# Optimization experiments

Measured on AMD Instinct MI355X. Metric: run time of the kernel, lower is better.

The kernel has to match this reference:

```python
import jax, jax.numpy as jnp
import numpy as np

GROUP = 64  # hardcoded group_size in the module


def setup_inputs() -> dict:
    key = jax.random.key(0)
    ks = jax.random.split(key, 7)
    B, S, K, N, R = 64, 1, 4096, 12288, 32
    G = K // GROUP
    x = jax.random.normal(ks[0], (B, S, K), jnp.float32)
    # int4 weight residual values in [-8, 7]
    q_w = jax.random.randint(ks[1], (N, K), -8, 8, jnp.int32)
    # per-(group, out_channel) positive scales, shape [G, N] as in the module buffer
    wscales = jax.random.uniform(ks[2], (G, N), jnp.float32, 1e-3, 2e-2)
    lora_down = jax.random.normal(ks[3], (K, R), jnp.float32) * 0.02
    lora_up = jax.random.normal(ks[4], (N, R), jnp.float32) * 0.02
    smooth = jax.random.uniform(ks[5], (K,), jnp.float32, 0.5, 2.0)
    bias = jax.random.normal(ks[6], (N,), jnp.float32) * 0.01
    return {"x": x, "q_w": q_w, "wscales": wscales, "lora_down": lora_down,
            "lora_up": lora_up, "smooth": smooth, "bias": bias}


def reference(x, q_w, wscales, lora_down, lora_up, smooth, bias):
    # x: [B, S, K]; q_w: [N, K] int4 values; wscales: [K//64, N]
    B, S, K = x.shape
    G = K // GROUP
    # smoothing divide (per in-channel)
    x_div = x / smooth  # [B, S, K]
    # --- activation W4A4 path: symmetric int4 per-token per-group quantization ---
    xg = x_div.reshape(B, S, G, GROUP)
    ascale = jnp.maximum(jnp.max(jnp.abs(xg), axis=-1) / 7.0, 1e-8)  # [B, S, G]
    xq = jnp.clip(jnp.round(xg / ascale[..., None]), -8.0, 7.0)
    x_deq = (xq * ascale[..., None]).reshape(B, S, K)  # dequantized activation
    # --- dequantize int4 weight residual: w[n,k] = q[n,k] * wscales[k//64, n] ---
    w_deq = q_w.astype(jnp.float32) * jnp.repeat(wscales, GROUP, axis=0).T  # [N, K]
    # main quantized GEMM
    y = jnp.einsum('bsk,nk->bsn', x_deq, w_deq)  # [B, S, N]
    # low-rank SVD branch on the full-precision smoothed activation
    y = y + (x_div @ lora_down) @ lora_up.T
    y = y + bias
    return y
```

## Files before the change

kernel.cpp:

```cpp
#include <hip/hip_runtime.h>
#include <hip/hip_bf16.h>

#define K_DIM 4096
#define N_DIM 12288
#define B_DIM 64
#define G_DIM 64
#define R_DIM 32
#define NT_DIM 768

typedef int v4i __attribute__((ext_vector_type(4)));

__device__ __forceinline__ int pack4(const v4i a) {
    return (a.x & 255) | ((a.y & 255) << 8) | ((a.z & 255) << 16) | (a.w << 24);
}

__global__ __launch_bounds__(256) void quant_lora_kernel(
    const float* __restrict__ x, const float* __restrict__ smooth,
    const float* __restrict__ ld, char* __restrict__ xq_p,
    float* __restrict__ ascale, float* __restrict__ t_part) {
    const int b = blockIdx.x >> 4;
    const int kc = blockIdx.x & 15;
    const int tid = threadIdx.x;
    const int k = kc * 256 + tid;

    __shared__ float sx[256];
    __shared__ float red[256];

    const float xd = x[b * K_DIM + k] / smooth[k];
    sx[tid] = xd;

    const int lane = tid & 63;
    float a = fabsf(xd);
    #pragma unroll
    for (int off = 32; off; off >>= 1) a = fmaxf(a, __shfl_xor(a, off));
    const float as = fmaxf(a / 7.0f, 1e-8f);
    float q = rintf(xd / as);
    q = fminf(fmaxf(q, -8.0f), 7.0f);
    const int g = kc * 4 + (tid >> 6);
    const int bt = b >> 4, b15 = b & 15;
    const int quad = lane >> 4, kin = lane & 15;
    xq_p[((((size_t)bt * G_DIM + g) * 64) + quad * 16 + b15) * 16 + kin] = (char)(int)q;
    if (lane == 0) ascale[b * G_DIM + g] = as;
    __syncthreads();

    const int r = tid & 31, c = tid >> 5;
    const int kb = kc * 256 + c * 32;
    float acc = 0.f;
    #pragma unroll 8
    for (int kk = 0; kk < 32; ++kk)
        acc += sx[c * 32 + kk] * ld[(size_t)(kb + kk) * R_DIM + r];
    red[tid] = acc;
    __syncthreads();
    if (tid < 32) {
        float s = 0.f;
        #pragma unroll
        for (int c2 = 0; c2 < 8; ++c2) s += red[c2 * 32 + tid];
        t_part[kc * (B_DIM * R_DIM) + b * R_DIM + tid] = s;
    }
}

__global__ __launch_bounds__(256) void main_fused_kernel(
    const int* __restrict__ qw, const float* __restrict__ wscales,
    const v4i* __restrict__ xq_p, const float* __restrict__ ascale,
    const float* __restrict__ t_part, const float* __restrict__ lora_up,
    const float* __restrict__ bias, float* __restrict__ out) {
    __shared__ float s_ws[G_DIM * 16];
    __shared__ float s_as[G_DIM * 68];
    __shared__ float s_t[B_DIM * R_DIM];

    const int nt = blockIdx.x;
    const int n0 = nt * 16;
    const int tid = threadIdx.x;

    for (int i = tid; i < G_DIM * 16; i += 256)
        s_ws[i] = wscales[(i >> 4) * N_DIM + n0 + (i & 15)];
    for (int i = tid; i < B_DIM * G_DIM; i += 256) {
        const int b = i >> 6, g = i & 63;
        s_as[g * 68 + b] = ascale[i];
    }
    for (int i = tid; i < B_DIM * R_DIM; i += 256) {
        float s = 0.f;
        #pragma unroll
        for (int kc = 0; kc < 16; ++kc) s += t_part[kc * (B_DIM * R_DIM) + i];
        s_t[i] = s;
    }
    __syncthreads();

    const int w = tid >> 6, lane = tid & 63;
    const int col = lane & 15, quad = lane >> 4;

    float facc[4] = {0.f, 0.f, 0.f, 0.f};
    const v4i zero = {0, 0, 0, 0};
    const v4i* xbase = xq_p + (size_t)w * G_DIM * 64 + lane;
    const int* bsrc = qw + (size_t)(n0 + col) * K_DIM + quad * 16;

    #pragma unroll 2
    for (int g = 0; g < G_DIM; ++g) {
        const int* p = bsrc + g * 64;
        const v4i a0 = *(const v4i*)(p);
        const v4i a1 = *(const v4i*)(p + 4);
        const v4i a2 = *(const v4i*)(p + 8);
        const v4i a3 = *(const v4i*)(p + 12);
        v4i bq;
        bq.x = pack4(a0); bq.y = pack4(a1); bq.z = pack4(a2); bq.w = pack4(a3);
        const v4i xa = xbase[g * 64];
        const v4i d = __builtin_amdgcn_mfma_i32_16x16x64_i8(xa, bq, zero, 0, 0, 0);
        const float wsc = s_ws[g * 16 + col];
        const float4 as4 = *(const float4*)&s_as[g * 68 + w * 16 + quad * 4];
        facc[0] = fmaf(as4.x * wsc, (float)d[0], facc[0]);
        facc[1] = fmaf(as4.y * wsc, (float)d[1], facc[1]);
        facc[2] = fmaf(as4.z * wsc, (float)d[2], facc[2]);
        facc[3] = fmaf(as4.w * wsc, (float)d[3], facc[3]);
    }

    const int n = n0 + col;
    float4 lu[8];
    {
        const float4* lp = (const float4*)(lora_up + (size_t)n * R_DIM);
        #pragma unroll
        for (int i = 0; i < 8; ++i) lu[i] = lp[i];
    }
    const float bs = bias[n];
    #pragma unroll
    for (int r = 0; r < 4; ++r) {
        const int b = w * 16 + quad * 4 + r;
        float acc = facc[r] + bs;
        #pragma unroll
        for (int r2 = 0; r2 < 8; ++r2) {
            const float4 tv = *(const float4*)&s_t[b * R_DIM + r2 * 4];
            acc += tv.x * lu[r2].x + tv.y * lu[r2].y +
                   tv.z * lu[r2].z + tv.w * lu[r2].w;
        }
        out[(size_t)b * N_DIM + n] = acc;
    }
}

extern "C" void kernel_launch(void* const* d_in, const int* in_sizes, int n_in,
                              void* d_out, int out_size, void* d_ws, size_t ws_size,
                              hipStream_t stream) {
    const float* x         = (const float*)d_in[0];
    const int*   q_w       = (const int*)d_in[1];
    const float* wscales   = (const float*)d_in[2];
    const float* lora_down = (const float*)d_in[3];
    const float* lora_up   = (const float*)d_in[4];
    const float* smooth    = (const float*)d_in[5];
    const float* bias      = (const float*)d_in[6];
    float* out = (float*)d_out;

    char*  xq     = (char*)d_ws;
    float* ascale = (float*)((char*)d_ws + 262144);
    float* t_part = (float*)((char*)d_ws + 262144 + 16384);

    quant_lora_kernel<<<B_DIM * 16, 256, 0, stream>>>(x, smooth, lora_down,
                                                      xq, ascale, t_part);
    main_fused_kernel<<<NT_DIM, 256, 0, stream>>>(q_w, wscales, (const v4i*)xq,
                                                  ascale, t_part, lora_up, bias, out);
}
```

Before: 327.3 us.

## Split main GEMM over K with partial-sum workspace and separate epilogue kernel

```diff
diff --git a/kernel.cpp b/kernel.cpp
--- a/kernel.cpp
+++ b/kernel.cpp
@@ -7,6 +7,7 @@
 #define G_DIM 64
 #define R_DIM 32
 #define NT_DIM 768
+#define GPB 16
 
 typedef int v4i __attribute__((ext_vector_type(4)));
 
@@ -59,30 +60,33 @@
     }
 }
 
-__global__ __launch_bounds__(256) void main_fused_kernel(
+__global__ __launch_bounds__(256) void treduce_kernel(
+    const float* __restrict__ t_part, float* __restrict__ t) {
+    const int i = blockIdx.x * 256 + threadIdx.x;
+    float s = 0.f;
+    #pragma unroll
+    for (int kc = 0; kc < 16; ++kc) s += t_part[kc * (B_DIM * R_DIM) + i];
+    t[i] = s;
+}
+
+__global__ __launch_bounds__(256) void main_ksplit_kernel(
     const int* __restrict__ qw, const float* __restrict__ wscales,
     const v4i* __restrict__ xq_p, const float* __restrict__ ascale,
-    const float* __restrict__ t_part, const float* __restrict__ lora_up,
-    const float* __restrict__ bias, float* __restrict__ out) {
-    __shared__ float s_ws[G_DIM * 16];
-    __shared__ float s_as[G_DIM * 68];
-    __shared__ float s_t[B_DIM * R_DIM];
+    float* __restrict__ psum) {
+    __shared__ float s_ws[GPB * 16];
+    __shared__ float s_as[GPB * 68];
 
-    const int nt = blockIdx.x;
-    const int n0 = nt * 16;
+    const int bid = blockIdx.x;
+    const int nt = bid >> 2, kc = bid & 3;
+    const int n0 = nt * 16, g0 = kc * GPB;
     const int tid = threadIdx.x;
 
-    for (int i = tid; i < G_DIM * 16; i += 256)
-        s_ws[i] = wscales[(i >> 4) * N_DIM + n0 + (i & 15)];
-    for (int i = tid; i < B_DIM * G_DIM; i += 256) {
-        const int b = i >> 6, g = i & 63;
-        s_as[g * 68 + b] = ascale[i];
-    }
-    for (int i = tid; i < B_DIM * R_DIM; i += 256) {
-        float s = 0.f;
-        #pragma unroll
-        for (int kc = 0; kc < 16; ++kc) s += t_part[kc * (B_DIM * R_DIM) + i];
-        s_t[i] = s;
+    if (tid < GPB * 16)
+        s_ws[tid] = wscales[(g0 + (tid >> 4)) * N_DIM + n0 + (tid & 15)];
+    #pragma unroll
+    for (int i = tid; i < B_DIM * GPB; i += 256) {
+        const int b = i & 63, gl = i >> 6;
+        s_as[gl * 68 + b] = ascale[b * G_DIM + g0 + gl];
     }
     __syncthreads();
 
@@ -95,7 +99,8 @@
     const int* bsrc = qw + (size_t)(n0 + col) * K_DIM + quad * 16;
 
     #pragma unroll 2
-    for (int g = 0; g < G_DIM; ++g) {
+    for (int gl = 0; gl < GPB; ++gl) {
+        const int g = g0 + gl;
         const int* p = bsrc + g * 64;
         const v4i a0 = *(const v4i*)(p);
         const v4i a1 = *(const v4i*)(p + 4);
@@ -103,17 +108,36 @@
         const v4i a3 = *(const v4i*)(p + 12);
         v4i bq;
         bq.x = pack4(a0); bq.y = pack4(a1); bq.z = pack4(a2); bq.w = pack4(a3);
-        const v4i xa = xbase[g * 64];
+        const v4i xa = xbase[(size_t)g * 64];
         const v4i d = __builtin_amdgcn_mfma_i32_16x16x64_i8(xa, bq, zero, 0, 0, 0);
-        const float wsc = s_ws[g * 16 + col];
-        const float4 as4 = *(const float4*)&s_as[g * 68 + w * 16 + quad * 4];
+        const float wsc = s_ws[gl * 16 + col];
+        const float4 as4 = *(const float4*)&s_as[gl * 68 + w * 16 + quad * 4];
         facc[0] = fmaf(as4.x * wsc, (float)d[0], facc[0]);
         facc[1] = fmaf(as4.y * wsc, (float)d[1], facc[1]);
         facc[2] = fmaf(as4.z * wsc, (float)d[2], facc[2]);
         facc[3] = fmaf(as4.w * wsc, (float)d[3], facc[3]);
     }
 
-    const int n = n0 + col;
+    float* pp = psum + (size_t)kc * B_DIM * N_DIM;
+    #pragma unroll
+    for (int r = 0; r < 4; ++r) {
+        const int b = w * 16 + quad * 4 + r;
+        pp[(size_t)b * N_DIM + n0 + col] = facc[r];
+    }
+}
+
+__global__ __launch_bounds__(256) void final_kernel(
+    const float* __restrict__ psum, const float* __restrict__ t,
+    const float* __restrict__ lora_up, const float* __restrict__ bias,
+    float* __restrict__ out) {
+    __shared__ float s_t[B_DIM * R_DIM];
+    const int n0 = blockIdx.x * 64;
+    const int tid = threadIdx.x;
+    for (int i = tid; i < B_DIM * R_DIM; i += 256) s_t[i] = t[i];
+    __syncthreads();
+
+    const int n = n0 + (tid & 63);
+    const int bq = tid >> 6;
     float4 lu[8];
     {
         const float4* lp = (const float4*)(lora_up + (size_t)n * R_DIM);
@@ -121,10 +145,13 @@
         for (int i = 0; i < 8; ++i) lu[i] = lp[i];
     }
     const float bs = bias[n];
-    #pragma unroll
-    for (int r = 0; r < 4; ++r) {
-        const int b = w * 16 + quad * 4 + r;
-        float acc = facc[r] + bs;
+    #pragma unroll 4
+    for (int r = 0; r < 16; ++r) {
+        const int b = bq * 16 + r;
+        float acc = bs;
+        #pragma unroll
+        for (int kc = 0; kc < 4; ++kc)
+            acc += psum[((size_t)kc * B_DIM + b) * N_DIM + n];
         #pragma unroll
         for (int r2 = 0; r2 < 8; ++r2) {
             const float4 tv = *(const float4*)&s_t[b * R_DIM + r2 * 4];
@@ -150,9 +177,14 @@
     char*  xq     = (char*)d_ws;
     float* ascale = (float*)((char*)d_ws + 262144);
     float* t_part = (float*)((char*)d_ws + 262144 + 16384);
+    float* t      = (float*)((char*)d_ws + 409600);
+    float* psum   = (float*)((char*)d_ws + 417792);
 
     quant_lora_kernel<<<B_DIM * 16, 256, 0, stream>>>(x, smooth, lora_down,
                                                       xq, ascale, t_part);
-    main_fused_kernel<<<NT_DIM, 256, 0, stream>>>(q_w, wscales, (const v4i*)xq,
-                                                  ascale, t_part, lora_up, bias, out);
+    treduce_kernel<<<8, 256, 0, stream>>>(t_part, t);
+    main_ksplit_kernel<<<NT_DIM * 4, 256, 0, stream>>>(q_w, wscales,
+                                                       (const v4i*)xq, ascale,
+                                                       psum);
+    final_kernel<<<N_DIM / 64, 256, 0, stream>>>(psum, t, lora_up, bias, out);
 }
```

Result: slower. 348.4 us (+6.5%).
